# Kernel optimization log

Hardware: AMD Instinct MI355X
Metric: run time of the kernel (lower is better)

The kernel has to match this reference:

```python
import jax, jax.numpy as jnp
import numpy as np

P = 9  # patch_size

def _conv3d(x, w, b):
    # x: (B,C,D,H,W), w: (O,I,3,3,3) -> SAME conv, stride 1
    out = jax.lax.conv_general_dilated(
        x, w, window_strides=(1, 1, 1), padding='SAME',
        dimension_numbers=('NCDHW', 'OIDHW', 'NCDHW'))
    return out + b[None, :, None, None, None]

def _unfold(z):
    # z: (C, D, HW) with D % P == 0 and HW % P == 0.
    # nn.Unfold(kernel=(P,P), stride=(P,P)) on a (1,1,D,HW) image is an exact
    # non-overlapping tiling -> pure reshape. Returns (C, L, P*P) with the
    # patch flattened row-major (kh, kw), matching torch's unfold layout.
    C, D, HW = z.shape
    z = z.reshape(C, D // P, P, HW // P, P)
    return z.transpose(0, 1, 3, 2, 4).reshape(C, (D // P) * (HW // P), P * P)

def _res_trans(t, W1, W2):
    # Linear(81->162, no bias) -> Linear(162->81, no bias) -> LeakyReLU(0.2)
    return jax.nn.leaky_relu(jnp.einsum('clk,ok->clo', jnp.einsum('clp,hp->clh', t, W1), W2), 0.2)

def setup_inputs() -> dict:
    key = jax.random.key(0)
    ks = jax.random.split(key, 8)
    B, C, D, H, W = 1, 32, 36, 48, 48
    s = 0.05
    return {
        'x':  jax.random.normal(ks[0], (B, C, D, H, W), jnp.float32),
        'y':  jax.random.normal(ks[1], (B, C, D, H, W), jnp.float32),
        'Wx': jax.random.normal(ks[2], (C, C, 3, 3, 3), jnp.float32) * s,
        'bx': jax.random.normal(ks[3], (C,), jnp.float32) * s,
        'Wy': jax.random.normal(ks[4], (C, C, 3, 3, 3), jnp.float32) * s,
        'by': jax.random.normal(ks[5], (C,), jnp.float32) * s,
        'W1': jax.random.normal(ks[6], (2 * P * P, P * P), jnp.float32) * s,
        'W2': jax.random.normal(ks[7], (P * P, 2 * P * P), jnp.float32) * s,
    }

def reference(x, y, Wx, bx, Wy, by, W1, W2):
    xc = _conv3d(x, Wx, bx)  # (1,C,D,H,W)
    yc = _conv3d(y, Wy, by)
    _, C, D, H, Wd = xc.shape
    xr = xc.reshape(C, D, H * Wd)
    yr = yc.reshape(C, D, H * Wd)
    a = _res_trans(_unfold(xr), W1, W2)  # (C, L, 81)
    b = _res_trans(_unfold(yr), W1, W2)  # (C, L, 81)
    # torch: matmul(unfold_img(L,81), trans(unfold_feamap).T(81,L)) / 81
    att = jnp.einsum('clp,cmp->clm', a, b) / (P * P)  # (C, L, L)
    return att[None]  # (1, C, L, L)
```

## Files before the change

kernel.cpp:

```cpp
#include <hip/hip_runtime.h>
#include <hip/hip_bf16.h>

typedef __attribute__((ext_vector_type(8))) short short8;
typedef __attribute__((ext_vector_type(4))) float f32x4;


static __device__ __forceinline__ unsigned short f2bf(float f) {
    unsigned int u = __float_as_uint(f);
    unsigned int r = (u + 0x7fffu + ((u >> 16) & 1u)) >> 16;
    return (unsigned short)r;
}

__global__ __launch_bounds__(256) void setup_kernel(
    const float* __restrict__ x, const float* __restrict__ y,
    const float* __restrict__ W1, const float* __restrict__ W2,
    const float* __restrict__ Wx, const float* __restrict__ Wy,
    unsigned short* __restrict__ xt, unsigned short* __restrict__ Mo,
    unsigned short* __restrict__ Wbf, unsigned short* __restrict__ tbuf) {
    int bb = blockIdx.x, tid = threadIdx.x;
    if (bb < 3800) {
        int img = bb / 1900, rr = bb % 1900;
        int dd = rr / 50, hh = rr % 50;
        unsigned short* dst = xt + img*(38*50*50*32) + (dd*50 + hh)*(50*32);
        if (dd >= 1 && dd <= 36 && hh >= 1 && hh <= 48) {
            __shared__ unsigned short lds[48*33];
            int d = dd - 1, h = hh - 1;
            const float* src = img ? y : x;
            for (int i = tid; i < 384; i += 256) {
                int ci = i / 12, w4 = (i % 12) * 4;
                float4 v = *reinterpret_cast<const float4*>(
                    &src[((ci*36 + d)*48 + h)*48 + w4]);
                lds[(w4+0)*33 + ci] = f2bf(v.x);
                lds[(w4+1)*33 + ci] = f2bf(v.y);
                lds[(w4+2)*33 + ci] = f2bf(v.z);
                lds[(w4+3)*33 + ci] = f2bf(v.w);
            }
            __syncthreads();
            #pragma unroll
            for (int i = 0; i < 7; ++i) {
                int idx = tid + 256*i;
                if (idx < 1600) {
                    int wp = idx >> 5, ci = idx & 31;
                    unsigned short v = (wp == 0 || wp == 49) ? (unsigned short)0
                                                             : lds[(wp-1)*33 + ci];
                    dst[idx] = v;
                }
            }
        } else {
            #pragma unroll
            for (int i = 0; i < 7; ++i) {
                int idx = tid + 256*i;
                if (idx < 1600) dst[idx] = 0;
            }
        }
    } else if (bb < 3836) {
        int gid = (bb - 3800)*256 + tid;
        int o = gid / 96, p = gid % 96;
        float v = 0.f;
        if (o < 81 && p < 81) {
            for (int k = 0; k < 162; ++k) v += W2[o*162 + k] * W1[k*81 + p];
        }
        Mo[o*96 + p] = f2bf(v);
    } else if (bb < 4052) {
        int e = (bb - 3836)*256 + tid;
        if (e < 2*27*32*32) {
            int ci  = e % 32;
            int co  = (e / 32) % 32;
            int tap = (e / 1024) % 27;
            int img = e / 27648;
            const float* src = img ? Wy : Wx;
            Wbf[e] = f2bf(src[co*864 + ci*27 + tap]);
        }
    } else {
        int row = (bb - 4052)*256 + tid;
        unsigned short* tr = tbuf + row*96 + 81;
        #pragma unroll
        for (int j = 0; j < 15; ++j) tr[j] = 0;
    }
}

__global__ __launch_bounds__(192, 1) void conv_kernel(
    const unsigned short* __restrict__ xt,
    const float* __restrict__ bx, const float* __restrict__ by,
    const unsigned short* __restrict__ Wbf, unsigned short* __restrict__ tbuf) {
    __shared__ __align__(16) float red[2][12][64][4];
    int b = blockIdx.x;
    int wg = (b & 7) * 216 + (b >> 3);
    int img = wg / 864; int rr = wg % 864;
    int d0 = rr / 24; int hp = rr % 24;
    int tid = threadIdx.x, kd = tid >> 6, lane = tid & 63;
    int r16 = lane & 15, g4 = lane >> 4;
    int hbase = hp*2;
    const unsigned short* Ximg = xt + img*(38*50*50*32);
    const unsigned short* Wimg = Wbf + img*(27*32*32);
    const float* bias = img ? by : bx;

    f32x4 acc[2][3][2];
    #pragma unroll
    for (int i = 0; i < 2; ++i)
        #pragma unroll
        for (int j = 0; j < 3; ++j)
            #pragma unroll
            for (int k = 0; k < 2; ++k) acc[i][j][k] = (f32x4){0.f, 0.f, 0.f, 0.f};

    short8 wf[3][3][2];
    #pragma unroll
    for (int kh = 0; kh < 3; ++kh)
        #pragma unroll
        for (int kw = 0; kw < 3; ++kw)
            #pragma unroll
            for (int ct = 0; ct < 2; ++ct)
                wf[kh][kw][ct] = *reinterpret_cast<const short8*>(
                    Wimg + (((kd*3 + kh)*3 + kw)*32 + ct*16 + r16)*32 + 8*g4);

    #pragma unroll
    for (int r = 0; r < 4; ++r) {
        const unsigned short* xrow = Ximg + ((d0 + kd)*50 + (hbase + r))*(50*32);
        #pragma unroll
        for (int kw = 0; kw < 3; ++kw) {
            short8 bfr[3];
            #pragma unroll
            for (int wt = 0; wt < 3; ++wt)
                bfr[wt] = *reinterpret_cast<const short8*>(xrow + (wt*16 + r16 + kw)*32 + 8*g4);
            #pragma unroll
            for (int hh = 0; hh < 2; ++hh) {
                int kh = r - hh;
                if (kh >= 0 && kh < 3) {
                    #pragma unroll
                    for (int wt = 0; wt < 3; ++wt) {
                        acc[0][wt][hh] = __builtin_amdgcn_mfma_f32_16x16x32_bf16(wf[kh][kw][0], bfr[wt], acc[0][wt][hh], 0, 0, 0);
                        acc[1][wt][hh] = __builtin_amdgcn_mfma_f32_16x16x32_bf16(wf[kh][kw][1], bfr[wt], acc[1][wt][hh], 0, 0, 0);
                    }
                }
            }
        }
    }

    #pragma unroll
    for (int ct = 0; ct < 2; ++ct)
        #pragma unroll
        for (int wt = 0; wt < 3; ++wt)
            #pragma unroll
            for (int hh = 0; hh < 2; ++hh) {
                int u = (ct*3 + wt)*2 + hh;
                int f = u >> 2;
                if (f != kd) {
                    int j = (kd - f + 2) % 3;
                    *reinterpret_cast<f32x4*>(&red[j][u][lane][0]) = acc[ct][wt][hh];
                }
            }
    __syncthreads();

    int l_hi = (d0/9)*256, p_hi = (d0%9)*9;
    unsigned short* tb = tbuf + img*(32*1024*96);
#define FIN(U, CT, WT, HH) { \
    f32x4 s = acc[CT][WT][HH] \
            + *reinterpret_cast<const f32x4*>(&red[0][U][lane][0]) \
            + *reinterpret_cast<const f32x4*>(&red[1][U][lane][0]); \
    int h = hbase + HH; \
    _Pragma("unroll") \
    for (int r = 0; r < 4; ++r) { \
        int co = CT*16 + g4*4 + r; \
        int w  = WT*16 + r16; \
        float v = s[r] + bias[co]; \
        int hw = h*48 + w; \
        int l = l_hi + hw/9, p = p_hi + hw%9; \
        tb[(co*1024 + l)*96 + p] = f2bf(v); \
    } }
    if (kd == 0)      { FIN(0,0,0,0) FIN(1,0,0,1) FIN(2,0,1,0)  FIN(3,0,1,1)  }
    else if (kd == 1) { FIN(4,0,2,0) FIN(5,0,2,1) FIN(6,1,0,0)  FIN(7,1,0,1)  }
    else              { FIN(8,1,1,0) FIN(9,1,1,1) FIN(10,1,2,0) FIN(11,1,2,1) }
#undef FIN
}

__global__ __launch_bounds__(256, 1) void rt_kernel(const unsigned short* __restrict__ tbuf,
                                                    const unsigned short* __restrict__ Mo,
                                                    unsigned short* __restrict__ ab) {
    int b = blockIdx.x;
    int img = b >> 7, c = (b >> 2) & 31, mc = b & 3;
    int tid = threadIdx.x, wv = tid >> 6, lane = tid & 63;
    int r16 = lane & 15, g4 = lane >> 4;

    short8 Bf[3][6];
    #pragma unroll
    for (int ks = 0; ks < 3; ++ks)
        #pragma unroll
        for (int n = 0; n < 6; ++n)
            Bf[ks][n] = *reinterpret_cast<const short8*>(Mo + (n*16 + r16)*96 + ks*32 + 8*g4);

    const unsigned short* tc = tbuf + (img*32 + c)*(1024*96);
    unsigned short*       oc = ab   + (img*32 + c)*(1024*96);
    for (int q = 0; q < 4; ++q) {
        int rowb = (mc*16 + wv*4 + q) * 16;
        f32x4 acc[6];
        #pragma unroll
        for (int n = 0; n < 6; ++n) acc[n] = (f32x4){0.f, 0.f, 0.f, 0.f};
        #pragma unroll
        for (int ks = 0; ks < 3; ++ks) {
            short8 Af = *reinterpret_cast<const short8*>(tc + (rowb + r16)*96 + ks*32 + 8*g4);
            #pragma unroll
            for (int n = 0; n < 6; ++n)
                acc[n] = __builtin_amdgcn_mfma_f32_16x16x32_bf16(Af, Bf[ks][n], acc[n], 0, 0, 0);
        }
        #pragma unroll
        for (int n = 0; n < 6; ++n)
            #pragma unroll
            for (int r = 0; r < 4; ++r) {
                int row = rowb + g4*4 + r;
                float v = acc[n][r];
                v = v > 0.f ? v : 0.2f*v;
                oc[row*96 + n*16 + r16] = f2bf(v);
            }
    }
}

__global__ __launch_bounds__(256) void att_kernel(const unsigned short* __restrict__ ab,
                                                  float* __restrict__ out) {
    int bid = blockIdx.x;
    int b = (bid & 7) * 256 + (bid >> 3);
    int c = b >> 6, ty = (b >> 3) & 7, tx = b & 7;
    int tid = threadIdx.x, wv = tid >> 6, lane = tid & 63;
    int r16 = lane & 15, g4 = lane >> 4;
    const unsigned short* arow = ab + c*(1024*96);
    const unsigned short* brow = ab + (32 + c)*(1024*96);
    int rb = ty*128 + wv*32;
    int cb = tx*128;
    f32x4 acc[2][8];
    #pragma unroll
    for (int m = 0; m < 2; ++m)
        #pragma unroll
        for (int n = 0; n < 8; ++n) acc[m][n] = (f32x4){0.f, 0.f, 0.f, 0.f};

    #pragma unroll
    for (int ks = 0; ks < 3; ++ks) {
        short8 A0 = *reinterpret_cast<const short8*>(arow + (rb +      r16)*96 + ks*32 + 8*g4);
        short8 A1 = *reinterpret_cast<const short8*>(arow + (rb + 16 + r16)*96 + ks*32 + 8*g4);
        #pragma unroll
        for (int n = 0; n < 8; ++n) {
            short8 Bf = *reinterpret_cast<const short8*>(brow + (cb + n*16 + r16)*96 + ks*32 + 8*g4);
            acc[0][n] = __builtin_amdgcn_mfma_f32_16x16x32_bf16(A0, Bf, acc[0][n], 0, 0, 0);
            acc[1][n] = __builtin_amdgcn_mfma_f32_16x16x32_bf16(A1, Bf, acc[1][n], 0, 0, 0);
        }
    }
    const float s = 1.f / 81.f;
    #pragma unroll
    for (int mt = 0; mt < 2; ++mt)
        #pragma unroll
        for (int n = 0; n < 8; ++n)
            #pragma unroll
            for (int r = 0; r < 4; ++r) {
                int row = rb + mt*16 + g4*4 + r;
                int col = cb + n*16 + r16;
                out[(c*1024 + row)*1024 + col] = acc[mt][n][r] * s;
            }
}

extern "C" void kernel_launch(void* const* d_in, const int* in_sizes, int n_in,
                              void* d_out, int out_size, void* d_ws, size_t ws_size,
                              hipStream_t stream) {
    const float* x  = (const float*)d_in[0];
    const float* y  = (const float*)d_in[1];
    const float* Wx = (const float*)d_in[2];
    const float* bx = (const float*)d_in[3];
    const float* Wy = (const float*)d_in[4];
    const float* by = (const float*)d_in[5];
    const float* W1 = (const float*)d_in[6];
    const float* W2 = (const float*)d_in[7];
    (void)in_sizes; (void)n_in; (void)out_size; (void)ws_size;

    char* ws = (char*)d_ws;
    unsigned short* xt   = (unsigned short*)(ws);
    unsigned short* abuf = (unsigned short*)(ws);
    unsigned short* tbuf = (unsigned short*)(ws + 12582912);
    unsigned short* Mo   = (unsigned short*)(ws + 25165824);
    unsigned short* Wbf  = (unsigned short*)(ws + 25184256);
    float* out = (float*)d_out;

    setup_kernel<<<4308, 256, 0, stream>>>(x, y, W1, W2, Wx, Wy, xt, Mo, Wbf, tbuf);
    conv_kernel<<<1728, 192, 0, stream>>>(xt, bx, by, Wbf, tbuf);
    rt_kernel<<<256, 256, 0, stream>>>(tbuf, Mo, abuf);
    att_kernel<<<2048, 256, 0, stream>>>(abuf, out);
}
```

Baseline: 79.62 us.

## Fuse res_trans projection into attention kernel via LDS staging

Removes the separate rt_kernel and its bf16 intermediate buffer. Each attention block now recomputes the leaky-ReLU projection for its 128-row A tile and 128-row B tile and stages both in padded shared memory, then runs the attention MFMA from LDS. This saves a kernel launch and a global round trip of the intermediate. In exchange, each A/B tile's projection is recomputed 8 times across blocks, and the kernel uses about 53KB of LDS per block, which can limit occupancy.

```diff
diff --git a/kernel.cpp b/kernel.cpp
--- a/kernel.cpp
+++ b/kernel.cpp
@@ -173,76 +173,80 @@
 #undef FIN
 }
 
-__global__ __launch_bounds__(256, 1) void rt_kernel(const unsigned short* __restrict__ tbuf,
-                                                    const unsigned short* __restrict__ Mo,
-                                                    unsigned short* __restrict__ ab) {
-    int b = blockIdx.x;
-    int img = b >> 7, c = (b >> 2) & 31, mc = b & 3;
-    int tid = threadIdx.x, wv = tid >> 6, lane = tid & 63;
-    int r16 = lane & 15, g4 = lane >> 4;
-
-    short8 Bf[3][6];
-    #pragma unroll
-    for (int ks = 0; ks < 3; ++ks)
-        #pragma unroll
-        for (int n = 0; n < 6; ++n)
-            Bf[ks][n] = *reinterpret_cast<const short8*>(Mo + (n*16 + r16)*96 + ks*32 + 8*g4);
-
-    const unsigned short* tc = tbuf + (img*32 + c)*(1024*96);
-    unsigned short*       oc = ab   + (img*32 + c)*(1024*96);
-    for (int q = 0; q < 4; ++q) {
-        int rowb = (mc*16 + wv*4 + q) * 16;
-        f32x4 acc[6];
-        #pragma unroll
-        for (int n = 0; n < 6; ++n) acc[n] = (f32x4){0.f, 0.f, 0.f, 0.f};
-        #pragma unroll
-        for (int ks = 0; ks < 3; ++ks) {
-            short8 Af = *reinterpret_cast<const short8*>(tc + (rowb + r16)*96 + ks*32 + 8*g4);
-            #pragma unroll
-            for (int n = 0; n < 6; ++n)
-                acc[n] = __builtin_amdgcn_mfma_f32_16x16x32_bf16(Af, Bf[ks][n], acc[n], 0, 0, 0);
-        }
-        #pragma unroll
-        for (int n = 0; n < 6; ++n)
-            #pragma unroll
-            for (int r = 0; r < 4; ++r) {
-                int row = rowb + g4*4 + r;
-                float v = acc[n][r];
-                v = v > 0.f ? v : 0.2f*v;
-                oc[row*96 + n*16 + r16] = f2bf(v);
-            }
-    }
-}
-
-__global__ __launch_bounds__(256) void att_kernel(const unsigned short* __restrict__ ab,
-                                                  float* __restrict__ out) {
+#define PST 104
+__global__ __launch_bounds__(256) void att2_kernel(
+    const unsigned short* __restrict__ tbuf,
+    const unsigned short* __restrict__ Mo,
+    float* __restrict__ out) {
+    __shared__ __align__(16) unsigned short a_lds[128][PST];
+    __shared__ __align__(16) unsigned short b_lds[128][PST];
     int bid = blockIdx.x;
     int b = (bid & 7) * 256 + (bid >> 3);
     int c = b >> 6, ty = (b >> 3) & 7, tx = b & 7;
     int tid = threadIdx.x, wv = tid >> 6, lane = tid & 63;
     int r16 = lane & 15, g4 = lane >> 4;
-    const unsigned short* arow = ab + c*(1024*96);
-    const unsigned short* brow = ab + (32 + c)*(1024*96);
+
+    short8 Bf[3][6];
+    #pragma unroll
+    for (int ks = 0; ks < 3; ++ks)
+        #pragma unroll
+        for (int n = 0; n < 6; ++n)
+            Bf[ks][n] = *reinterpret_cast<const short8*>(Mo + (n*16 + r16)*96 + ks*32 + 8*g4);
+
+    const unsigned short* ta = tbuf + c*(1024*96);
+    const unsigned short* tbp = tbuf + (32 + c)*(1024*96);
+    #pragma unroll
+    for (int half = 0; half < 2; ++half) {
+        const unsigned short* tc = half ? tbp : ta;
+        int gbase = (half ? tx : ty)*128 + wv*32;
+        unsigned short (*lds)[PST] = half ? b_lds : a_lds;
+        #pragma unroll
+        for (int q = 0; q < 2; ++q) {
+            int rowg = gbase + q*16;
+            int rowl = wv*32 + q*16;
+            f32x4 acc[6];
+            #pragma unroll
+            for (int n = 0; n < 6; ++n) acc[n] = (f32x4){0.f, 0.f, 0.f, 0.f};
+            #pragma unroll
+            for (int ks = 0; ks < 3; ++ks) {
+                short8 Af = *reinterpret_cast<const short8*>(tc + (rowg + r16)*96 + ks*32 + 8*g4);
+                #pragma unroll
+                for (int n = 0; n < 6; ++n)
+                    acc[n] = __builtin_amdgcn_mfma_f32_16x16x32_bf16(Af, Bf[ks][n], acc[n], 0, 0, 0);
+            }
+            #pragma unroll
+            for (int n = 0; n < 6; ++n)
+                #pragma unroll
+                for (int r = 0; r < 4; ++r) {
+                    float v = acc[n][r];
+                    v = v > 0.f ? v : 0.2f*v;
+                    lds[rowl + g4*4 + r][n*16 + r16] = f2bf(v);
+                }
+        }
+    }
+    __syncthreads();
+
+    int rbl = wv*32;
+    f32x4 acc[2][8];
+    #pragma unroll
+    for (int m = 0; m < 2; ++m)
+        #pragma unroll
+        for (int n = 0; n < 8; ++n) acc[m][n] = (f32x4){0.f, 0.f, 0.f, 0.f};
+
+    #pragma unroll
+    for (int ks = 0; ks < 3; ++ks) {
+        short8 A0 = *reinterpret_cast<const short8*>(&a_lds[rbl +      r16][ks*32 + 8*g4]);
+        short8 A1 = *reinterpret_cast<const short8*>(&a_lds[rbl + 16 + r16][ks*32 + 8*g4]);
+        #pragma unroll
+        for (int n = 0; n < 8; ++n) {
+            short8 Bp = *reinterpret_cast<const short8*>(&b_lds[n*16 + r16][ks*32 + 8*g4]);
+            acc[0][n] = __builtin_amdgcn_mfma_f32_16x16x32_bf16(A0, Bp, acc[0][n], 0, 0, 0);
+            acc[1][n] = __builtin_amdgcn_mfma_f32_16x16x32_bf16(A1, Bp, acc[1][n], 0, 0, 0);
+        }
+    }
+    const float s = 1.f / 81.f;
     int rb = ty*128 + wv*32;
     int cb = tx*128;
-    f32x4 acc[2][8];
-    #pragma unroll
-    for (int m = 0; m < 2; ++m)
-        #pragma unroll
-        for (int n = 0; n < 8; ++n) acc[m][n] = (f32x4){0.f, 0.f, 0.f, 0.f};
-
-    #pragma unroll
-    for (int ks = 0; ks < 3; ++ks) {
-        short8 A0 = *reinterpret_cast<const short8*>(arow + (rb +      r16)*96 + ks*32 + 8*g4);
-        short8 A1 = *reinterpret_cast<const short8*>(arow + (rb + 16 + r16)*96 + ks*32 + 8*g4);
-        #pragma unroll
-        for (int n = 0; n < 8; ++n) {
-            short8 Bf = *reinterpret_cast<const short8*>(brow + (cb + n*16 + r16)*96 + ks*32 + 8*g4);
-            acc[0][n] = __builtin_amdgcn_mfma_f32_16x16x32_bf16(A0, Bf, acc[0][n], 0, 0, 0);
-            acc[1][n] = __builtin_amdgcn_mfma_f32_16x16x32_bf16(A1, Bf, acc[1][n], 0, 0, 0);
-        }
-    }
-    const float s = 1.f / 81.f;
     #pragma unroll
     for (int mt = 0; mt < 2; ++mt)
         #pragma unroll
@@ -254,6 +258,7 @@
                 out[(c*1024 + row)*1024 + col] = acc[mt][n][r] * s;
             }
 }
+#undef PST
 
 extern "C" void kernel_launch(void* const* d_in, const int* in_sizes, int n_in,
                               void* d_out, int out_size, void* d_ws, size_t ws_size,
@@ -270,7 +275,6 @@
 
     char* ws = (char*)d_ws;
     unsigned short* xt   = (unsigned short*)(ws);
-    unsigned short* abuf = (unsigned short*)(ws);
     unsigned short* tbuf = (unsigned short*)(ws + 12582912);
     unsigned short* Mo   = (unsigned short*)(ws + 25165824);
     unsigned short* Wbf  = (unsigned short*)(ws + 25184256);
@@ -278,6 +282,5 @@
 
     setup_kernel<<<4308, 256, 0, stream>>>(x, y, W1, W2, Wx, Wy, xt, Mo, Wbf, tbuf);
     conv_kernel<<<1728, 192, 0, stream>>>(xt, bx, by, Wbf, tbuf);
-    rt_kernel<<<256, 256, 0, stream>>>(tbuf, Mo, abuf);
-    att_kernel<<<2048, 256, 0, stream>>>(abuf, out);
-}
+    att2_kernel<<<2048, 256, 0, stream>>>(tbuf, Mo, out);
+}
```

Result: slower. 81.67 us (+2.6%).
